# Performance work log

Measured on AMD Instinct MI355X. Metric: run time of the kernel, lower is better.

## Reference

```python
import jax, jax.numpy as jnp
import numpy as np

N, E, DIN, DOUT = 50000, 800000, 256, 256
P = DOUT // 2  # attention projection dim = feature_dim // 2


def _mlp2(x, W1, b1, W2, b2):
    # nn.Sequential(Linear, ReLU, Linear)
    return jax.nn.relu(x @ W1 + b1) @ W2 + b2


def _spmm(indices, values, x):
    # y[r] = sum_e values[e] * x[col[e]] for edges with row[e] == r
    rows, cols = indices[0], indices[1]
    return jax.ops.segment_sum(values[:, None] * x[cols], rows, num_segments=x.shape[0])


def setup_inputs() -> dict:
    key = jax.random.key(0)
    ks = iter(jax.random.split(key, 64))

    def nrm(shape, scale=0.05):
        return jax.random.normal(next(ks), shape, jnp.float32) * scale

    inp = {}
    inp["features"] = jax.random.normal(next(ks), (N, DIN), jnp.float32)
    inp["edge_features"] = jax.random.normal(next(ks), (N, DOUT), jnp.float32)
    for i in (1, 2, 3, 4):
        inp[f"adj{i}_indices"] = jax.random.randint(next(ks), (2, E), 0, N)
        inp[f"adj{i}_values"] = jax.random.uniform(next(ks), (E,), jnp.float32)
    # feature_transform: Linear(in, out)
    inp["ft_W"] = nrm((DIN, DOUT)); inp["ft_b"] = jnp.zeros((DOUT,), jnp.float32)
    # six 2-layer MLPs: first_order(fo), edge(em), second(so), third(to), fourth(qo), final(m)
    for p in ("fo", "em", "so", "to", "qo", "m"):
        inp[f"{p}_W1"] = nrm((DOUT, DOUT)); inp[f"{p}_b1"] = jnp.zeros((DOUT,), jnp.float32)
        inp[f"{p}_W2"] = nrm((DOUT, DOUT)); inp[f"{p}_b2"] = jnp.zeros((DOUT,), jnp.float32)
    # attention query/key projections to DOUT//2
    inp["q_W"] = nrm((DOUT, P)); inp["q_b"] = jnp.zeros((P,), jnp.float32)
    inp["k_W"] = nrm((DOUT, P)); inp["k_b"] = jnp.zeros((P,), jnp.float32)
    return inp


def reference(features, edge_features,
              adj1_indices, adj1_values, adj2_indices, adj2_values,
              adj3_indices, adj3_values, adj4_indices, adj4_values,
              ft_W, ft_b,
              fo_W1, fo_b1, fo_W2, fo_b2,
              em_W1, em_b1, em_W2, em_b2,
              so_W1, so_b1, so_W2, so_b2,
              to_W1, to_b1, to_W2, to_b2,
              qo_W1, qo_b1, qo_W2, qo_b2,
              m_W1, m_b1, m_W2, m_b2,
              q_W, q_b, k_W, k_b):
    feats = features @ ft_W + ft_b                                    # [N, DOUT]
    # first order: spmm -> MLP, then add spmm of edge-MLP features
    fo = _mlp2(_spmm(adj1_indices, adj1_values, feats), fo_W1, fo_b1, fo_W2, fo_b2)
    ef = _mlp2(edge_features, em_W1, em_b1, em_W2, em_b2)
    fo = fo + _spmm(adj1_indices, adj1_values, ef)
    # higher orders: spmm -> MLP + residual
    so_agg = _spmm(adj2_indices, adj2_values, feats)
    so = _mlp2(so_agg, so_W1, so_b1, so_W2, so_b2) + so_agg
    to_agg = _spmm(adj3_indices, adj3_values, feats)
    to = _mlp2(to_agg, to_W1, to_b1, to_W2, to_b2) + to_agg
    qo_agg = _spmm(adj4_indices, adj4_values, feats)
    qo = _mlp2(qo_agg, qo_W1, qo_b1, qo_W2, qo_b2) + qo_agg
    # attention combination over the 5 feature sets
    all_f = jnp.stack([feats, fo, so, to, qo], axis=1)                # [N, 5, DOUT]
    q = feats @ q_W + q_b                                             # [N, P]
    keys = all_f @ k_W + k_b                                          # [N, 5, P]
    scores = jnp.einsum('np,nkp->nk', q, keys)                        # [N, 5]
    w = jax.nn.softmax(scores, axis=-1)
    combined = jnp.einsum('nk,nkd->nd', w, all_f)                     # [N, DOUT]
    # final MLP (dropout is identity in eval mode)
    return _mlp2(combined, m_W1, m_b1, m_W2, m_b2)
```

## Files before the change

kernel.cpp:

```cpp
#include <hip/hip_runtime.h>


#define DO 256

typedef unsigned short u16;
typedef _Float16 f16;
typedef __attribute__((ext_vector_type(8))) _Float16 f16x8;
typedef __attribute__((ext_vector_type(4))) _Float16 f16x4;
typedef __attribute__((ext_vector_type(4))) float f32x4;


struct WDesc { const float* src; f16* dst; };
struct WPack { WDesc w[13]; };

__global__ __launch_bounds__(256) void transpose_w_kernel(WPack p) {
    WDesc d = p.w[blockIdx.y];
    int idx = blockIdx.x * 256 + threadIdx.x;
    int e  = idx & 7;
    int l  = (idx >> 3) & 63;
    int ks = (idx >> 9) & 7;
    int f  = idx >> 12;
    int c  = (f << 4) | (l & 15);
    int k  = ks * 32 + ((l >> 4) << 3) + e;
    d.dst[idx] = (f16)d.src[k * 256 + c];
}

__global__ __launch_bounds__(256) void build_p_kernel(
    const float* __restrict__ qW, const float* __restrict__ kW,
    f16* __restrict__ pdst)
{
    int idx = blockIdx.x * 256 + threadIdx.x;
    int e  = idx & 7;
    int l  = (idx >> 3) & 63;
    int ks = (idx >> 9) & 7;
    int f  = idx >> 12;
    int c  = (f << 4) | (l & 15);
    int k  = ks * 32 + ((l >> 4) << 3) + e;
    float s = 0.f;
    #pragma unroll 8
    for (int p = 0; p < 128; ++p) s += qW[k * 128 + p] * kW[c * 128 + p];
    pdst[idx] = (f16)s;
}

__global__ __launch_bounds__(256) void build_pb_kernel(
    const float* __restrict__ qb, const float* __restrict__ kW,
    float* __restrict__ pb)
{
    int c = threadIdx.x;
    float s = 0.f;
    #pragma unroll 8
    for (int p = 0; p < 128; ++p) s += qb[p] * kW[c * 128 + p];
    pb[c] = s;
}

static __device__ __forceinline__ void stage_A(
    char* smem, const f16* A, const float* A32, int brow, int N, int tid)
{
    #pragma unroll
    for (int j = 0; j < 8; ++j) {
        int i = tid + j * 256;
        int row = i >> 5, slot = i & 31;
        int srow = brow + row; srow = srow < N ? srow : N - 1;
        f16x8 v;
        if (A32) {
            const float* s = &A32[(size_t)srow * 256 + slot * 8];
            float4 v0 = *(const float4*)s;
            float4 v1 = *(const float4*)(s + 4);
            v = f16x8{(f16)v0.x, (f16)v0.y, (f16)v0.z, (f16)v0.w,
                      (f16)v1.x, (f16)v1.y, (f16)v1.z, (f16)v1.w};
        } else {
            v = *(const f16x8*)&A[(size_t)srow * 256 + slot * 8];
        }
        int db = (row * 512 + slot * 16) ^ ((row & 7) << 4);
        *(f16x8*)(smem + db) = v;
    }
}

static __device__ __forceinline__ void gemm_from_lds(
    const char* smem, const f16* W, f32x4 (&acc)[4][4],
    int wave, int lane, int lrow, int kg)
{
    #pragma unroll
    for (int ks = 0; ks < 8; ++ks) {
        f16x8 ah[4], bh[4];
        #pragma unroll
        for (int m = 0; m < 4; ++m) {
            int ab = ((m * 16 + lrow) * 512 + (ks * 4 + kg) * 16) ^ ((lrow & 7) << 4);
            ah[m] = *(const f16x8*)(smem + ab);
        }
        #pragma unroll
        for (int n = 0; n < 4; ++n)
            bh[n] = *(const f16x8*)&W[(size_t)(((wave * 4 + n) * 8 + ks) << 9) + (lane << 3)];
        #pragma unroll
        for (int m = 0; m < 4; ++m)
            #pragma unroll
            for (int n = 0; n < 4; ++n)
                acc[m][n] = __builtin_amdgcn_mfma_f32_16x16x32_f16(
                                ah[m], bh[n], acc[m][n], 0, 0, 0);
    }
}

static __device__ __forceinline__ void fused_mlp_body(
    char* smem, const f16* A, const float* A32,
    const f16* W1, const float* b1, const f16* W2, const float* b2,
    const f16* Ad, f16* Ch, float* Cf, int N, int brow)
{
    const int tid  = threadIdx.x;
    const int wave = tid >> 6, lane = tid & 63;
    const int lrow = lane & 15, kg = lane >> 4;
    const int wc   = wave * 64;

    stage_A(smem, A, A32, brow, N, tid);
    __syncthreads();

    f32x4 acc[4][4] = {};
    gemm_from_lds(smem, W1, acc, wave, lane, lrow, kg);

    __syncthreads();
    #pragma unroll
    for (int n = 0; n < 4; ++n) {
        int c = wc + n * 16 + lrow;
        float bv = b1[c];
        #pragma unroll
        for (int m = 0; m < 4; ++m)
            #pragma unroll
            for (int j = 0; j < 4; ++j) {
                int rl = m * 16 + kg * 4 + j;
                float v = fmaxf(acc[m][n][j] + bv, 0.f);
                int hb = (rl * 512 + c * 2) ^ ((rl & 7) << 4);
                *(f16*)(smem + hb) = (f16)v;
            }
    }
    __syncthreads();

    #pragma unroll
    for (int m = 0; m < 4; ++m)
        #pragma unroll
        for (int n = 0; n < 4; ++n)
            acc[m][n] = f32x4{0.f, 0.f, 0.f, 0.f};
    gemm_from_lds(smem, W2, acc, wave, lane, lrow, kg);

    #pragma unroll
    for (int n = 0; n < 4; ++n) {
        int c = wc + n * 16 + lrow;
        float bv = b2[c];
        #pragma unroll
        for (int m = 0; m < 4; ++m)
            #pragma unroll
            for (int j = 0; j < 4; ++j) {
                int r = brow + m * 16 + kg * 4 + j;
                if (r >= N) continue;
                size_t o = (size_t)r * 256 + c;
                float v = acc[m][n][j] + bv;
                if (Ad) v += (float)Ad[o];
                if (Cf) Cf[o] = v;
                else    Ch[o] = (f16)v;
            }
    }
}

__global__ __launch_bounds__(256) void gemm1_kernel(
    const float* __restrict__ A32, const f16* __restrict__ W1,
    const float* __restrict__ b1, f16* __restrict__ Ch, int N)
{
    __shared__ char smem[32768];
    const int tid  = threadIdx.x;
    const int wave = tid >> 6, lane = tid & 63;
    const int lrow = lane & 15, kg = lane >> 4;
    const int wc   = wave * 64;
    const int brow = blockIdx.x * 64;

    stage_A(smem, nullptr, A32, brow, N, tid);
    __syncthreads();
    f32x4 acc[4][4] = {};
    gemm_from_lds(smem, W1, acc, wave, lane, lrow, kg);

    #pragma unroll
    for (int n = 0; n < 4; ++n) {
        int c = wc + n * 16 + lrow;
        float bv = b1[c];
        #pragma unroll
        for (int m = 0; m < 4; ++m)
            #pragma unroll
            for (int j = 0; j < 4; ++j) {
                int r = brow + m * 16 + kg * 4 + j;
                if (r >= N) continue;
                acc[m][n][j] += bv;
                Ch[(size_t)r * 256 + c] = (f16)acc[m][n][j];
            }
    }
}

__global__ __launch_bounds__(256) void mlp_kernel(
    const f16* __restrict__ A, const float* __restrict__ A32,
    const f16* __restrict__ W1, const float* __restrict__ b1,
    const f16* __restrict__ W2, const float* __restrict__ b2,
    const f16* __restrict__ Ad, f16* __restrict__ Ch, float* __restrict__ Cf,
    int N)
{
    __shared__ char smem[32768];
    fused_mlp_body(smem, A, A32, W1, b1, W2, b2, Ad, Ch, Cf, N, blockIdx.x * 64);
}

struct Mlp4 {
    const f16* a[4]; const f16* ad[4];
    const f16* w1[4]; const f16* w2[4];
    const float* b1[4]; const float* b2[4];
    f16* out[4];
};
__global__ __launch_bounds__(256) void mlp4_kernel(Mlp4 p, int N) {
    __shared__ char smem[32768];
    int y = blockIdx.y;
    fused_mlp_body(smem, p.a[y], nullptr, p.w1[y], p.b1[y], p.w2[y], p.b2[y],
                   p.ad[y], p.out[y], nullptr, N, blockIdx.x * 64);
}

__global__ __launch_bounds__(256) void score_combine_kernel(
    const f16* __restrict__ F, const f16* __restrict__ P,
    const float* __restrict__ pb,
    const f16* __restrict__ F1, const f16* __restrict__ F2,
    const f16* __restrict__ F3, const f16* __restrict__ F4,
    f16* __restrict__ O, int N)
{
    __shared__ char smem[32768];
    __shared__ float sred[4][64][5];
    __shared__ float w5[64][5];

    const int tid  = threadIdx.x;
    const int wave = tid >> 6, lane = tid & 63;
    const int lrow = lane & 15, kg = lane >> 4;
    const int wc   = wave * 64;
    const int brow = blockIdx.x * 64;

    stage_A(smem, F, nullptr, brow, N, tid);
    __syncthreads();

    f32x4 acc[4][4] = {};
    gemm_from_lds(smem, P, acc, wave, lane, lrow, kg);

    #pragma unroll
    for (int m = 0; m < 4; ++m) {
        #pragma unroll
        for (int j = 0; j < 4; ++j) {
            int rl = m * 16 + kg * 4 + j;
            int r  = brow + rl;
            float p0 = 0.f, p1 = 0.f, p2 = 0.f, p3 = 0.f, p4 = 0.f;
            if (r < N) {
                #pragma unroll
                for (int n = 0; n < 4; ++n) {
                    int c = wc + n * 16 + lrow;
                    float v = acc[m][n][j] + pb[c];
                    int ab = (rl * 512 + c * 2) ^ ((rl & 7) << 4);
                    float f0 = (float)*(const f16*)(smem + ab);
                    size_t fo = (size_t)r * 256 + c;
                    p0 += v * f0;
                    p1 += v * (float)F1[fo];
                    p2 += v * (float)F2[fo];
                    p3 += v * (float)F3[fo];
                    p4 += v * (float)F4[fo];
                }
            }
            #pragma unroll
            for (int d = 1; d < 16; d <<= 1) {
                p0 += __shfl_xor(p0, d, 64);
                p1 += __shfl_xor(p1, d, 64);
                p2 += __shfl_xor(p2, d, 64);
                p3 += __shfl_xor(p3, d, 64);
                p4 += __shfl_xor(p4, d, 64);
            }
            if (lrow == 0) {
                sred[wave][rl][0] = p0; sred[wave][rl][1] = p1;
                sred[wave][rl][2] = p2; sred[wave][rl][3] = p3;
                sred[wave][rl][4] = p4;
            }
        }
    }
    __syncthreads();

    if (tid < 64) {
        float s[5];
        #pragma unroll
        for (int k = 0; k < 5; ++k)
            s[k] = sred[0][tid][k] + sred[1][tid][k] + sred[2][tid][k] + sred[3][tid][k];
        float mx = fmaxf(fmaxf(fmaxf(s[0], s[1]), fmaxf(s[2], s[3])), s[4]);
        float sum = 0.f;
        #pragma unroll
        for (int k = 0; k < 5; ++k) { s[k] = expf(s[k] - mx); sum += s[k]; }
        float inv = 1.f / sum;
        #pragma unroll
        for (int k = 0; k < 5; ++k) w5[tid][k] = s[k] * inv;
    }
    __syncthreads();

    #pragma unroll
    for (int m = 0; m < 4; ++m) {
        #pragma unroll
        for (int j = 0; j < 4; ++j) {
            int rl = m * 16 + kg * 4 + j;
            int r  = brow + rl;
            if (r >= N) continue;
            float w0 = w5[rl][0], w1 = w5[rl][1], w2 = w5[rl][2],
                  w3 = w5[rl][3], w4 = w5[rl][4];
            #pragma unroll
            for (int n = 0; n < 4; ++n) {
                int c = wc + n * 16 + lrow;
                int ab = (rl * 512 + c * 2) ^ ((rl & 7) << 4);
                float f0 = (float)*(const f16*)(smem + ab);
                size_t fo = (size_t)r * 256 + c;
                float res = w0 * f0
                          + w1 * (float)F1[fo]
                          + w2 * (float)F2[fo]
                          + w3 * (float)F3[fo]
                          + w4 * (float)F4[fo];
                O[fo] = (f16)res;
            }
        }
    }
}

struct CsrSrc { const int* rows[4]; const int* cols[4]; const float* vals[4]; int E[4]; };

__global__ __launch_bounds__(256) void count4_kernel(CsrSrc s, int* __restrict__ cnt, int NPo) {
    int a = blockIdx.y;
    int e = blockIdx.x * 256 + threadIdx.x;
    if (e < s.E[a]) atomicAdd(&cnt[(size_t)a * NPo + s.rows[a][e]], 1);
}

__global__ __launch_bounds__(1024) void scan4_kernel(
    const int* __restrict__ cnt0, int* __restrict__ off0, int N, int NPo)
{
    const int* cnt = cnt0 + (size_t)blockIdx.x * NPo;
    int* off = off0 + (size_t)blockIdx.x * NPo;
    __shared__ int part[1024];
    const int t = threadIdx.x;
    const int chunk = (N + 1023) / 1024;
    const int lo = t * chunk;
    const int hi = min(lo + chunk, N);
    int s = 0;
    for (int i = lo; i < hi; ++i) s += cnt[i];
    part[t] = s;
    __syncthreads();
    for (int d = 1; d < 1024; d <<= 1) {
        int u = (t >= d) ? part[t - d] : 0;
        __syncthreads();
        part[t] += u;
        __syncthreads();
    }
    int running = part[t] - s;
    for (int i = lo; i < hi; ++i) { off[i] = running; running += cnt[i]; }
    if (t == 1023) off[N] = part[1023];
}

__global__ __launch_bounds__(256) void scatter4_kernel(
    CsrSrc s, const int* __restrict__ off, int* __restrict__ cur,
    int2* __restrict__ se, int NPo, int Emax)
{
    int a = blockIdx.y;
    int e = blockIdx.x * 256 + threadIdx.x;
    if (e >= s.E[a]) return;
    int r = s.rows[a][e];
    int p = off[(size_t)a * NPo + r] + atomicAdd(&cur[(size_t)a * NPo + r], 1);
    se[(size_t)a * Emax + p] = make_int2(s.cols[a][e],
                                         __float_as_int(s.vals[a][e]));
}

struct Spmm4 {
    const int* off; const int2* se; int NPo; int Emax;
    const f16* F; const f16* ef;
    f16* agg1; f16* aggef; f16* agg2; f16* agg3; f16* agg4;
};
__global__ __launch_bounds__(256) void spmm4_kernel(Spmm4 s, int N) {
    int a = blockIdx.y;
    int r = blockIdx.x * 4 + (threadIdx.x >> 6);
    if (r >= N) return;
    int lane = threadIdx.x & 63;
    const int* off = s.off + (size_t)a * s.NPo;
    const int2* se = s.se + (size_t)a * s.Emax;
    int e0 = off[r], e1 = off[r + 1];
    size_t yo = (size_t)r * DO + lane * 4;

    if (a == 0) {
        float a0 = 0.f, a1 = 0.f, a2 = 0.f, a3 = 0.f;
        float b0 = 0.f, b1 = 0.f, b2 = 0.f, b3 = 0.f;
        for (int e = e0; e < e1; ++e) {
            int2 ev = se[e];
            int c = ev.x; float v = __int_as_float(ev.y);
            size_t xo = (size_t)c * DO + lane * 4;
            f16x4 x1 = *(const f16x4*)&s.F[xo];
            f16x4 x2 = *(const f16x4*)&s.ef[xo];
            a0 = fmaf(v, (float)x1[0], a0); a1 = fmaf(v, (float)x1[1], a1);
            a2 = fmaf(v, (float)x1[2], a2); a3 = fmaf(v, (float)x1[3], a3);
            b0 = fmaf(v, (float)x2[0], b0); b1 = fmaf(v, (float)x2[1], b1);
            b2 = fmaf(v, (float)x2[2], b2); b3 = fmaf(v, (float)x2[3], b3);
        }
        f16x4 o1 = {(f16)a0, (f16)a1, (f16)a2, (f16)a3};
        f16x4 o2 = {(f16)b0, (f16)b1, (f16)b2, (f16)b3};
        *(f16x4*)&s.agg1[yo]  = o1;
        *(f16x4*)&s.aggef[yo] = o2;
    } else {
        f16* Y = (a == 1) ? s.agg2 : (a == 2) ? s.agg3 : s.agg4;
        float a0 = 0.f, a1 = 0.f, a2 = 0.f, a3 = 0.f;
        for (int e = e0; e < e1; ++e) {
            int2 ev = se[e];
            int c = ev.x; float v = __int_as_float(ev.y);
            f16x4 x = *(const f16x4*)&s.F[(size_t)c * DO + lane * 4];
            a0 = fmaf(v, (float)x[0], a0); a1 = fmaf(v, (float)x[1], a1);
            a2 = fmaf(v, (float)x[2], a2); a3 = fmaf(v, (float)x[3], a3);
        }
        f16x4 o = {(f16)a0, (f16)a1, (f16)a2, (f16)a3};
        *(f16x4*)&Y[yo] = o;
    }
}

extern "C" void kernel_launch(void* const* d_in, const int* in_sizes, int n_in,
                              void* d_out, int out_size, void* d_ws, size_t ws_size,
                              hipStream_t stream)
{
    const float* features      = (const float*)d_in[0];
    const float* edge_features = (const float*)d_in[1];
    CsrSrc cs;
    for (int i = 0; i < 4; ++i) {
        const int* idx = (const int*)d_in[2 + 2 * i];
        cs.E[i]    = in_sizes[3 + 2 * i];
        cs.rows[i] = idx;
        cs.cols[i] = idx + cs.E[i];
        cs.vals[i] = (const float*)d_in[3 + 2 * i];
    }
    const int Emax = max(max(cs.E[0], cs.E[1]), max(cs.E[2], cs.E[3]));

    const float* ft_W = (const float*)d_in[10]; const float* ft_b = (const float*)d_in[11];
    const float* fo_W1 = (const float*)d_in[12]; const float* fo_b1 = (const float*)d_in[13];
    const float* fo_W2 = (const float*)d_in[14]; const float* fo_b2 = (const float*)d_in[15];
    const float* em_W1 = (const float*)d_in[16]; const float* em_b1 = (const float*)d_in[17];
    const float* em_W2 = (const float*)d_in[18]; const float* em_b2 = (const float*)d_in[19];
    const float* so_W1 = (const float*)d_in[20]; const float* so_b1 = (const float*)d_in[21];
    const float* so_W2 = (const float*)d_in[22]; const float* so_b2 = (const float*)d_in[23];
    const float* to_W1 = (const float*)d_in[24]; const float* to_b1 = (const float*)d_in[25];
    const float* to_W2 = (const float*)d_in[26]; const float* to_b2 = (const float*)d_in[27];
    const float* qo_W1 = (const float*)d_in[28]; const float* qo_b1 = (const float*)d_in[29];
    const float* qo_W2 = (const float*)d_in[30]; const float* qo_b2 = (const float*)d_in[31];
    const float* m_W1  = (const float*)d_in[32]; const float* m_b1  = (const float*)d_in[33];
    const float* m_W2  = (const float*)d_in[34]; const float* m_b2  = (const float*)d_in[35];
    const float* q_W   = (const float*)d_in[36]; const float* q_b   = (const float*)d_in[37];
    const float* k_W   = (const float*)d_in[38]; const float* k_b   = (const float*)d_in[39];
    (void)k_b;

    const int N = in_sizes[0] / 256;
    const size_t NS = (size_t)N * DO;

    char* base = (char*)d_ws;
    size_t o = 0;
    auto take = [&](size_t bytes) { char* p = base + o; o += (bytes + 63) & ~(size_t)63; return p; };
    const int NPo = (N + 64) & ~63;
    int*  cnt = (int*)take((size_t)4 * NPo * 4);
    int*  cur = (int*)take((size_t)4 * NPo * 4);
    int*  off = (int*)take((size_t)4 * NPo * 4);
    int2* se  = (int2*)take((size_t)4 * Emax * 8);
    f16* B1 = (f16*)take(NS * 2);
    f16* B2 = (f16*)take(NS * 2);
    f16* B3 = (f16*)take(NS * 2);
    f16* B4 = (f16*)take(NS * 2);
    f16* B5 = (f16*)take(NS * 2);
    f16* B6 = (f16*)take(NS * 2);
    const size_t WSQ = 65536;
    f16* WT = (f16*)take(14 * WSQ * 2);
    float* pb = (float*)take(256 * 4);
    if (o > ws_size) return;

    f16* F  = B4;
    f16* OT = (f16*)d_out;

    f16* w[14];
    for (int i = 0; i < 14; ++i) w[i] = WT + (size_t)i * WSQ;

    dim3 blk(256);
    {
        WPack p;
        const float* src[13] = {ft_W, fo_W1, fo_W2, em_W1, em_W2, so_W1, so_W2,
                                to_W1, to_W2, qo_W1, qo_W2, m_W1, m_W2};
        for (int i = 0; i < 13; ++i) { p.w[i].src = src[i]; p.w[i].dst = w[i]; }
        hipLaunchKernelGGL(transpose_w_kernel, dim3(256, 13), blk, 0, stream, p);
    }
    hipLaunchKernelGGL(build_p_kernel, dim3(256), blk, 0, stream, q_W, k_W, w[13]);
    hipLaunchKernelGGL(build_pb_kernel, dim3(1), blk, 0, stream, q_b, k_W, pb);
    {
        hipMemsetAsync(cnt, 0, (size_t)4 * NPo * 4, stream);
        hipMemsetAsync(cur, 0, (size_t)4 * NPo * 4, stream);
        dim3 egrd((Emax + 255) / 256, 4);
        hipLaunchKernelGGL(count4_kernel, egrd, blk, 0, stream, cs, cnt, NPo);
        hipLaunchKernelGGL(scan4_kernel, dim3(4), dim3(1024), 0, stream, cnt, off, N, NPo);
        hipLaunchKernelGGL(scatter4_kernel, egrd, blk, 0, stream, cs, off, cur, se, NPo, Emax);
    }

    dim3 ggrd((N + 63) / 64);
    dim3 rgrd((N + 3) / 4);

    hipLaunchKernelGGL(gemm1_kernel, ggrd, blk, 0, stream, features, w[0], ft_b, F, N);
    hipLaunchKernelGGL(mlp_kernel, ggrd, blk, 0, stream,
                       nullptr, edge_features, w[3], em_b1, w[4], em_b2,
                       nullptr, B3, nullptr, N);
    {
        Spmm4 sp;
        sp.off = off; sp.se = se; sp.NPo = NPo; sp.Emax = Emax;
        sp.F = F; sp.ef = B3;
        sp.agg1 = B1; sp.aggef = B2; sp.agg2 = B5; sp.agg3 = B6; sp.agg4 = OT;
        hipLaunchKernelGGL(spmm4_kernel, dim3((N + 3) / 4, 4), blk, 0, stream, sp, N);
    }
    {
        Mlp4 p;
        const f16* a[4]  = {B1, B5, B6, OT};
        const f16* ad[4] = {B2, B5, B6, OT};
        f16* out[4]      = {B1, B5, B6, OT};
        int wi1[4] = {1, 5, 7, 9}, wi2[4] = {2, 6, 8, 10};
        const float* bb1[4] = {fo_b1, so_b1, to_b1, qo_b1};
        const float* bb2[4] = {fo_b2, so_b2, to_b2, qo_b2};
        for (int i = 0; i < 4; ++i) {
            p.a[i] = a[i]; p.ad[i] = ad[i]; p.out[i] = out[i];
            p.w1[i] = w[wi1[i]]; p.w2[i] = w[wi2[i]];
            p.b1[i] = bb1[i]; p.b2[i] = bb2[i];
        }
        hipLaunchKernelGGL(mlp4_kernel, dim3((N + 63) / 64, 4), blk, 0, stream, p, N);
    }
    hipLaunchKernelGGL(score_combine_kernel, ggrd, blk, 0, stream,
                       F, w[13], pb, B1, B5, B6, OT, B1, N);
    hipLaunchKernelGGL(mlp_kernel, ggrd, blk, 0, stream,
                       B1, nullptr, w[11], m_b1, w[12], m_b2,
                       nullptr, nullptr, (float*)d_out, N);
}
```

Before: 1.194 ms.

## Fuse preprocessing kernels into combined prep and stage2 launches

Merges CSR counting, weight transposes and attention projection prep into one multi-role kernel. CSR scatter, the feature GEMM and the edge MLP are combined into a second kernel so independent work runs concurrently. The two memsets are replaced by one. The spmm loop for the higher-order adjacencies is unrolled by two to overlap gathers. This reduces launch count and serialization, at the cost of many idle early-exit blocks in the oversized grids.

```diff
diff --git a/kernel.cpp b/kernel.cpp
--- a/kernel.cpp
+++ b/kernel.cpp
@@ -12,45 +12,78 @@
 
 struct WDesc { const float* src; f16* dst; };
 struct WPack { WDesc w[13]; };
-
-__global__ __launch_bounds__(256) void transpose_w_kernel(WPack p) {
-    WDesc d = p.w[blockIdx.y];
-    int idx = blockIdx.x * 256 + threadIdx.x;
-    int e  = idx & 7;
-    int l  = (idx >> 3) & 63;
-    int ks = (idx >> 9) & 7;
-    int f  = idx >> 12;
-    int c  = (f << 4) | (l & 15);
-    int k  = ks * 32 + ((l >> 4) << 3) + e;
-    d.dst[idx] = (f16)d.src[k * 256 + c];
-}
-
-__global__ __launch_bounds__(256) void build_p_kernel(
+struct CsrSrc { const int* rows[4]; const int* cols[4]; const float* vals[4]; int E[4]; };
+
+__global__ __launch_bounds__(256) void prep_kernel(
+    CsrSrc cs, int* __restrict__ cnt, int NPo, WPack wp,
     const float* __restrict__ qW, const float* __restrict__ kW,
-    f16* __restrict__ pdst)
-{
-    int idx = blockIdx.x * 256 + threadIdx.x;
-    int e  = idx & 7;
-    int l  = (idx >> 3) & 63;
-    int ks = (idx >> 9) & 7;
-    int f  = idx >> 12;
-    int c  = (f << 4) | (l & 15);
-    int k  = ks * 32 + ((l >> 4) << 3) + e;
-    float s = 0.f;
-    #pragma unroll 8
-    for (int p = 0; p < 128; ++p) s += qW[k * 128 + p] * kW[c * 128 + p];
-    pdst[idx] = (f16)s;
-}
-
-__global__ __launch_bounds__(256) void build_pb_kernel(
-    const float* __restrict__ qb, const float* __restrict__ kW,
-    float* __restrict__ pb)
-{
+    const float* __restrict__ qb, f16* __restrict__ pdst, float* __restrict__ pb)
+{
+    int y = blockIdx.y;
+    if (y < 4) {
+        int e = blockIdx.x * 256 + threadIdx.x;
+        if (e < cs.E[y]) atomicAdd(&cnt[(size_t)y * NPo + cs.rows[y][e]], 1);
+        return;
+    }
+    if (y < 17) {
+        if (blockIdx.x >= 256) return;
+        WDesc d = wp.w[y - 4];
+        int idx = blockIdx.x * 256 + threadIdx.x;
+        int e  = idx & 7;
+        int l  = (idx >> 3) & 63;
+        int ks = (idx >> 9) & 7;
+        int f  = idx >> 12;
+        int c  = (f << 4) | (l & 15);
+        int k  = ks * 32 + ((l >> 4) << 3) + e;
+        d.dst[idx] = (f16)d.src[k * 256 + c];
+        return;
+    }
+    if (y == 17) {
+        if (blockIdx.x >= 256) return;
+        int idx = blockIdx.x * 256 + threadIdx.x;
+        int e  = idx & 7;
+        int l  = (idx >> 3) & 63;
+        int ks = (idx >> 9) & 7;
+        int f  = idx >> 12;
+        int c  = (f << 4) | (l & 15);
+        int k  = ks * 32 + ((l >> 4) << 3) + e;
+        float s = 0.f;
+        #pragma unroll 8
+        for (int p = 0; p < 128; ++p) s += qW[k * 128 + p] * kW[c * 128 + p];
+        pdst[idx] = (f16)s;
+        return;
+    }
+    if (blockIdx.x != 0) return;
     int c = threadIdx.x;
     float s = 0.f;
     #pragma unroll 8
     for (int p = 0; p < 128; ++p) s += qb[p] * kW[c * 128 + p];
     pb[c] = s;
+}
+
+__global__ __launch_bounds__(1024) void scan4_kernel(
+    const int* __restrict__ cnt0, int* __restrict__ off0, int N, int NPo)
+{
+    const int* cnt = cnt0 + (size_t)blockIdx.x * NPo;
+    int* off = off0 + (size_t)blockIdx.x * NPo;
+    __shared__ int part[1024];
+    const int t = threadIdx.x;
+    const int chunk = (N + 1023) / 1024;
+    const int lo = t * chunk;
+    const int hi = min(lo + chunk, N);
+    int s = 0;
+    for (int i = lo; i < hi; ++i) s += cnt[i];
+    part[t] = s;
+    __syncthreads();
+    for (int d = 1; d < 1024; d <<= 1) {
+        int u = (t >= d) ? part[t - d] : 0;
+        __syncthreads();
+        part[t] += u;
+        __syncthreads();
+    }
+    int running = part[t] - s;
+    for (int i = lo; i < hi; ++i) { off[i] = running; running += cnt[i]; }
+    if (t == 1023) off[N] = part[1023];
 }
 
 static __device__ __forceinline__ void stage_A(
@@ -159,16 +192,14 @@
     }
 }
 
-__global__ __launch_bounds__(256) void gemm1_kernel(
-    const float* __restrict__ A32, const f16* __restrict__ W1,
-    const float* __restrict__ b1, f16* __restrict__ Ch, int N)
-{
-    __shared__ char smem[32768];
+static __device__ __forceinline__ void gemm1_body(
+    char* smem, const float* A32, const f16* W1, const float* b1,
+    f16* Ch, int N, int brow)
+{
     const int tid  = threadIdx.x;
     const int wave = tid >> 6, lane = tid & 63;
     const int lrow = lane & 15, kg = lane >> 4;
     const int wc   = wave * 64;
-    const int brow = blockIdx.x * 64;
 
     stage_A(smem, nullptr, A32, brow, N, tid);
     __syncthreads();
@@ -185,21 +216,97 @@
             for (int j = 0; j < 4; ++j) {
                 int r = brow + m * 16 + kg * 4 + j;
                 if (r >= N) continue;
-                acc[m][n][j] += bv;
-                Ch[(size_t)r * 256 + c] = (f16)acc[m][n][j];
-            }
-    }
-}
-
-__global__ __launch_bounds__(256) void mlp_kernel(
-    const f16* __restrict__ A, const float* __restrict__ A32,
-    const f16* __restrict__ W1, const float* __restrict__ b1,
-    const f16* __restrict__ W2, const float* __restrict__ b2,
-    const f16* __restrict__ Ad, f16* __restrict__ Ch, float* __restrict__ Cf,
-    int N)
+                Ch[(size_t)r * 256 + c] = (f16)(acc[m][n][j] + bv);
+            }
+    }
+}
+
+__global__ __launch_bounds__(256) void stage2_kernel(
+    CsrSrc cs, const int* __restrict__ off, int* __restrict__ cur,
+    int2* __restrict__ se, int NPo, int Emax,
+    const float* __restrict__ features, const float* __restrict__ edge_features,
+    const f16* __restrict__ w_ft, const float* __restrict__ ft_b,
+    const f16* __restrict__ w_em1, const float* __restrict__ em_b1,
+    const f16* __restrict__ w_em2, const float* __restrict__ em_b2,
+    f16* __restrict__ F, f16* __restrict__ ef, int N)
 {
     __shared__ char smem[32768];
-    fused_mlp_body(smem, A, A32, W1, b1, W2, b2, Ad, Ch, Cf, N, blockIdx.x * 64);
+    int y = blockIdx.y;
+    if (y < 4) {
+        int e = blockIdx.x * 256 + threadIdx.x;
+        if (e >= cs.E[y]) return;
+        int r = cs.rows[y][e];
+        int p = off[(size_t)y * NPo + r] + atomicAdd(&cur[(size_t)y * NPo + r], 1);
+        se[(size_t)y * Emax + p] = make_int2(cs.cols[y][e],
+                                             __float_as_int(cs.vals[y][e]));
+        return;
+    }
+    int gx = blockIdx.x;
+    if (gx >= (N + 63) / 64) return;
+    if (y == 4)
+        gemm1_body(smem, features, w_ft, ft_b, F, N, gx * 64);
+    else
+        fused_mlp_body(smem, nullptr, edge_features, w_em1, em_b1, w_em2, em_b2,
+                       nullptr, ef, nullptr, N, gx * 64);
+}
+
+struct Spmm4 {
+    const int* off; const int2* se; int NPo; int Emax;
+    const f16* F; const f16* ef;
+    f16* agg1; f16* aggef; f16* agg2; f16* agg3; f16* agg4;
+};
+__global__ __launch_bounds__(256) void spmm4_kernel(Spmm4 s, int N) {
+    int a = blockIdx.y;
+    int r = blockIdx.x * 4 + (threadIdx.x >> 6);
+    if (r >= N) return;
+    int lane = threadIdx.x & 63;
+    const int* off = s.off + (size_t)a * s.NPo;
+    const int2* se = s.se + (size_t)a * s.Emax;
+    int e0 = off[r], e1 = off[r + 1];
+    size_t yo = (size_t)r * DO + lane * 4;
+
+    if (a == 0) {
+        float a0 = 0.f, a1 = 0.f, a2 = 0.f, a3 = 0.f;
+        float b0 = 0.f, b1 = 0.f, b2 = 0.f, b3 = 0.f;
+        for (int e = e0; e < e1; ++e) {
+            int2 ev = se[e];
+            int c = ev.x; float v = __int_as_float(ev.y);
+            size_t xo = (size_t)c * DO + lane * 4;
+            f16x4 x1 = *(const f16x4*)&s.F[xo];
+            f16x4 x2 = *(const f16x4*)&s.ef[xo];
+            a0 = fmaf(v, (float)x1[0], a0); a1 = fmaf(v, (float)x1[1], a1);
+            a2 = fmaf(v, (float)x1[2], a2); a3 = fmaf(v, (float)x1[3], a3);
+            b0 = fmaf(v, (float)x2[0], b0); b1 = fmaf(v, (float)x2[1], b1);
+            b2 = fmaf(v, (float)x2[2], b2); b3 = fmaf(v, (float)x2[3], b3);
+        }
+        f16x4 o1 = {(f16)a0, (f16)a1, (f16)a2, (f16)a3};
+        f16x4 o2 = {(f16)b0, (f16)b1, (f16)b2, (f16)b3};
+        *(f16x4*)&s.agg1[yo]  = o1;
+        *(f16x4*)&s.aggef[yo] = o2;
+    } else {
+        f16* Y = (a == 1) ? s.agg2 : (a == 2) ? s.agg3 : s.agg4;
+        float a0 = 0.f, a1 = 0.f, a2 = 0.f, a3 = 0.f;
+        int e = e0;
+        for (; e + 1 < e1; e += 2) {
+            int2 ev0 = se[e], ev1 = se[e + 1];
+            float v0 = __int_as_float(ev0.y), v1 = __int_as_float(ev1.y);
+            f16x4 x0 = *(const f16x4*)&s.F[(size_t)ev0.x * DO + lane * 4];
+            f16x4 x1 = *(const f16x4*)&s.F[(size_t)ev1.x * DO + lane * 4];
+            a0 = fmaf(v0, (float)x0[0], a0); a1 = fmaf(v0, (float)x0[1], a1);
+            a2 = fmaf(v0, (float)x0[2], a2); a3 = fmaf(v0, (float)x0[3], a3);
+            a0 = fmaf(v1, (float)x1[0], a0); a1 = fmaf(v1, (float)x1[1], a1);
+            a2 = fmaf(v1, (float)x1[2], a2); a3 = fmaf(v1, (float)x1[3], a3);
+        }
+        if (e < e1) {
+            int2 ev = se[e];
+            float v = __int_as_float(ev.y);
+            f16x4 x = *(const f16x4*)&s.F[(size_t)ev.x * DO + lane * 4];
+            a0 = fmaf(v, (float)x[0], a0); a1 = fmaf(v, (float)x[1], a1);
+            a2 = fmaf(v, (float)x[2], a2); a3 = fmaf(v, (float)x[3], a3);
+        }
+        f16x4 o = {(f16)a0, (f16)a1, (f16)a2, (f16)a3};
+        *(f16x4*)&Y[yo] = o;
+    }
 }
 
 struct Mlp4 {
@@ -213,6 +320,17 @@
     int y = blockIdx.y;
     fused_mlp_body(smem, p.a[y], nullptr, p.w1[y], p.b1[y], p.w2[y], p.b2[y],
                    p.ad[y], p.out[y], nullptr, N, blockIdx.x * 64);
+}
+
+__global__ __launch_bounds__(256) void mlp_kernel(
+    const f16* __restrict__ A,
+    const f16* __restrict__ W1, const float* __restrict__ b1,
+    const f16* __restrict__ W2, const float* __restrict__ b2,
+    float* __restrict__ Cf, int N)
+{
+    __shared__ char smem[32768];
+    fused_mlp_body(smem, A, nullptr, W1, b1, W2, b2, nullptr, nullptr, Cf, N,
+                   blockIdx.x * 64);
 }
 
 __global__ __launch_bounds__(256) void score_combine_kernel(
@@ -318,100 +436,6 @@
     }
 }
 
-struct CsrSrc { const int* rows[4]; const int* cols[4]; const float* vals[4]; int E[4]; };
-
-__global__ __launch_bounds__(256) void count4_kernel(CsrSrc s, int* __restrict__ cnt, int NPo) {
-    int a = blockIdx.y;
-    int e = blockIdx.x * 256 + threadIdx.x;
-    if (e < s.E[a]) atomicAdd(&cnt[(size_t)a * NPo + s.rows[a][e]], 1);
-}
-
-__global__ __launch_bounds__(1024) void scan4_kernel(
-    const int* __restrict__ cnt0, int* __restrict__ off0, int N, int NPo)
-{
-    const int* cnt = cnt0 + (size_t)blockIdx.x * NPo;
-    int* off = off0 + (size_t)blockIdx.x * NPo;
-    __shared__ int part[1024];
-    const int t = threadIdx.x;
-    const int chunk = (N + 1023) / 1024;
-    const int lo = t * chunk;
-    const int hi = min(lo + chunk, N);
-    int s = 0;
-    for (int i = lo; i < hi; ++i) s += cnt[i];
-    part[t] = s;
-    __syncthreads();
-    for (int d = 1; d < 1024; d <<= 1) {
-        int u = (t >= d) ? part[t - d] : 0;
-        __syncthreads();
-        part[t] += u;
-        __syncthreads();
-    }
-    int running = part[t] - s;
-    for (int i = lo; i < hi; ++i) { off[i] = running; running += cnt[i]; }
-    if (t == 1023) off[N] = part[1023];
-}
-
-__global__ __launch_bounds__(256) void scatter4_kernel(
-    CsrSrc s, const int* __restrict__ off, int* __restrict__ cur,
-    int2* __restrict__ se, int NPo, int Emax)
-{
-    int a = blockIdx.y;
-    int e = blockIdx.x * 256 + threadIdx.x;
-    if (e >= s.E[a]) return;
-    int r = s.rows[a][e];
-    int p = off[(size_t)a * NPo + r] + atomicAdd(&cur[(size_t)a * NPo + r], 1);
-    se[(size_t)a * Emax + p] = make_int2(s.cols[a][e],
-                                         __float_as_int(s.vals[a][e]));
-}
-
-struct Spmm4 {
-    const int* off; const int2* se; int NPo; int Emax;
-    const f16* F; const f16* ef;
-    f16* agg1; f16* aggef; f16* agg2; f16* agg3; f16* agg4;
-};
-__global__ __launch_bounds__(256) void spmm4_kernel(Spmm4 s, int N) {
-    int a = blockIdx.y;
-    int r = blockIdx.x * 4 + (threadIdx.x >> 6);
-    if (r >= N) return;
-    int lane = threadIdx.x & 63;
-    const int* off = s.off + (size_t)a * s.NPo;
-    const int2* se = s.se + (size_t)a * s.Emax;
-    int e0 = off[r], e1 = off[r + 1];
-    size_t yo = (size_t)r * DO + lane * 4;
-
-    if (a == 0) {
-        float a0 = 0.f, a1 = 0.f, a2 = 0.f, a3 = 0.f;
-        float b0 = 0.f, b1 = 0.f, b2 = 0.f, b3 = 0.f;
-        for (int e = e0; e < e1; ++e) {
-            int2 ev = se[e];
-            int c = ev.x; float v = __int_as_float(ev.y);
-            size_t xo = (size_t)c * DO + lane * 4;
-            f16x4 x1 = *(const f16x4*)&s.F[xo];
-            f16x4 x2 = *(const f16x4*)&s.ef[xo];
-            a0 = fmaf(v, (float)x1[0], a0); a1 = fmaf(v, (float)x1[1], a1);
-            a2 = fmaf(v, (float)x1[2], a2); a3 = fmaf(v, (float)x1[3], a3);
-            b0 = fmaf(v, (float)x2[0], b0); b1 = fmaf(v, (float)x2[1], b1);
-            b2 = fmaf(v, (float)x2[2], b2); b3 = fmaf(v, (float)x2[3], b3);
-        }
-        f16x4 o1 = {(f16)a0, (f16)a1, (f16)a2, (f16)a3};
-        f16x4 o2 = {(f16)b0, (f16)b1, (f16)b2, (f16)b3};
-        *(f16x4*)&s.agg1[yo]  = o1;
-        *(f16x4*)&s.aggef[yo] = o2;
-    } else {
-        f16* Y = (a == 1) ? s.agg2 : (a == 2) ? s.agg3 : s.agg4;
-        float a0 = 0.f, a1 = 0.f, a2 = 0.f, a3 = 0.f;
-        for (int e = e0; e < e1; ++e) {
-            int2 ev = se[e];
-            int c = ev.x; float v = __int_as_float(ev.y);
-            f16x4 x = *(const f16x4*)&s.F[(size_t)c * DO + lane * 4];
-            a0 = fmaf(v, (float)x[0], a0); a1 = fmaf(v, (float)x[1], a1);
-            a2 = fmaf(v, (float)x[2], a2); a3 = fmaf(v, (float)x[3], a3);
-        }
-        f16x4 o = {(f16)a0, (f16)a1, (f16)a2, (f16)a3};
-        *(f16x4*)&Y[yo] = o;
-    }
-}
-
 extern "C" void kernel_launch(void* const* d_in, const int* in_sizes, int n_in,
                               void* d_out, int out_size, void* d_ws, size_t ws_size,
                               hipStream_t stream)
@@ -474,31 +498,24 @@
     for (int i = 0; i < 14; ++i) w[i] = WT + (size_t)i * WSQ;
 
     dim3 blk(256);
+    const int EG = (Emax + 255) / 256;
+    const int GG = (N + 63) / 64;
+
+    hipMemsetAsync(cnt, 0, (size_t)8 * NPo * 4, stream);
+
     {
-        WPack p;
+        WPack wp;
         const float* src[13] = {ft_W, fo_W1, fo_W2, em_W1, em_W2, so_W1, so_W2,
                                 to_W1, to_W2, qo_W1, qo_W2, m_W1, m_W2};
-        for (int i = 0; i < 13; ++i) { p.w[i].src = src[i]; p.w[i].dst = w[i]; }
-        hipLaunchKernelGGL(transpose_w_kernel, dim3(256, 13), blk, 0, stream, p);
-    }
-    hipLaunchKernelGGL(build_p_kernel, dim3(256), blk, 0, stream, q_W, k_W, w[13]);
-    hipLaunchKernelGGL(build_pb_kernel, dim3(1), blk, 0, stream, q_b, k_W, pb);
-    {
-        hipMemsetAsync(cnt, 0, (size_t)4 * NPo * 4, stream);
-        hipMemsetAsync(cur, 0, (size_t)4 * NPo * 4, stream);
-        dim3 egrd((Emax + 255) / 256, 4);
-        hipLaunchKernelGGL(count4_kernel, egrd, blk, 0, stream, cs, cnt, NPo);
-        hipLaunchKernelGGL(scan4_kernel, dim3(4), dim3(1024), 0, stream, cnt, off, N, NPo);
-        hipLaunchKernelGGL(scatter4_kernel, egrd, blk, 0, stream, cs, off, cur, se, NPo, Emax);
-    }
-
-    dim3 ggrd((N + 63) / 64);
-    dim3 rgrd((N + 3) / 4);
-
-    hipLaunchKernelGGL(gemm1_kernel, ggrd, blk, 0, stream, features, w[0], ft_b, F, N);
-    hipLaunchKernelGGL(mlp_kernel, ggrd, blk, 0, stream,
-                       nullptr, edge_features, w[3], em_b1, w[4], em_b2,
-                       nullptr, B3, nullptr, N);
+        for (int i = 0; i < 13; ++i) { wp.w[i].src = src[i]; wp.w[i].dst = w[i]; }
+        hipLaunchKernelGGL(prep_kernel, dim3(EG, 19), blk, 0, stream,
+                           cs, cnt, NPo, wp, q_W, k_W, q_b, w[13], pb);
+    }
+    hipLaunchKernelGGL(scan4_kernel, dim3(4), dim3(1024), 0, stream, cnt, off, N, NPo);
+    hipLaunchKernelGGL(stage2_kernel, dim3(EG, 6), blk, 0, stream,
+                       cs, off, cur, se, NPo, Emax,
+                       features, edge_features,
+                       w[0], ft_b, w[3], em_b1, w[4], em_b2, F, B3, N);
     {
         Spmm4 sp;
         sp.off = off; sp.se = se; sp.NPo = NPo; sp.Emax = Emax;
@@ -519,11 +536,10 @@
             p.w1[i] = w[wi1[i]]; p.w2[i] = w[wi2[i]];
             p.b1[i] = bb1[i]; p.b2[i] = bb2[i];
         }
-        hipLaunchKernelGGL(mlp4_kernel, dim3((N + 63) / 64, 4), blk, 0, stream, p, N);
-    }
-    hipLaunchKernelGGL(score_combine_kernel, ggrd, blk, 0, stream,
+        hipLaunchKernelGGL(mlp4_kernel, dim3(GG, 4), blk, 0, stream, p, N);
+    }
+    hipLaunchKernelGGL(score_combine_kernel, dim3(GG), blk, 0, stream,
                        F, w[13], pb, B1, B5, B6, OT, B1, N);
-    hipLaunchKernelGGL(mlp_kernel, ggrd, blk, 0, stream,
-                       B1, nullptr, w[11], m_b1, w[12], m_b2,
-                       nullptr, nullptr, (float*)d_out, N);
-}
+    hipLaunchKernelGGL(mlp_kernel, dim3(GG), blk, 0, stream,
+                       B1, w[11], m_b1, w[12], m_b2, (float*)d_out, N);
+}
```

After: 1.112 ms. -6.9%, faster.
